# Performance work log

Measured on AMD Instinct MI355X. Metric: run time of the kernel, lower is better.

The kernel has to match this reference:

```python
import jax, jax.numpy as jnp
import numpy as np

NUM_EMBEDDINGS = 8192
EMBEDDING_DIM = 512
COMMITMENT_COST = 0.25


def setup_inputs() -> dict:
    key = jax.random.key(0)
    kz, ke = jax.random.split(key)
    z = jax.random.normal(kz, (2, EMBEDDING_DIM, 8, 32, 32), dtype=jnp.float32)
    # matches nn.Embedding init uniform_(-1/K, 1/K)
    emb_w = jax.random.uniform(
        ke, (NUM_EMBEDDINGS, EMBEDDING_DIM), dtype=jnp.float32,
        minval=-1.0 / NUM_EMBEDDINGS, maxval=1.0 / NUM_EMBEDDINGS)
    return {"z": z, "emb_w": emb_w}


def reference(z, emb_w):
    B, C, F, H, W = z.shape
    # [B,C,F,H,W] -> [N, C]
    z_flat = jnp.transpose(z, (0, 2, 3, 4, 1)).reshape(-1, C)
    # squared L2 distances via expansion: |z|^2 + |e|^2 - 2 z.e
    dist = (jnp.sum(z_flat * z_flat, axis=1, keepdims=True)
            + jnp.sum(emb_w * emb_w, axis=1)
            - 2.0 * jnp.matmul(z_flat, emb_w.T))  # [N, K]
    indices = jnp.argmin(dist, axis=1)  # [N]
    z_q_flat = emb_w[indices]  # [N, C]
    z_q = jnp.transpose(z_q_flat.reshape(B, F, H, W, C), (0, 4, 1, 2, 3))
    diff = z_q - z
    mse = jnp.mean(diff * diff)
    # codebook_loss == commitment_loss numerically (detach only affects grads)
    vq_loss = mse + COMMITMENT_COST * mse
    # straight-through estimator: value equals z_q
    z_q_ste = z + jax.lax.stop_gradient(z_q - z)
    indices = indices.reshape(B, F, H, W)
    return (z_q_ste, vq_loss, indices)
```

## Files before the change

kernel.cpp:

```cpp
#include <hip/hip_runtime.h>


constexpr int KCB = 8192;
constexpr int CD  = 512;
constexpr int SD  = 8192;
constexpr int NB  = 2;
constexpr int NR  = NB * SD;
constexpr long ZQ_ELEMS = (long)NB * CD * SD;

constexpr size_t WS_CNT   = 64;
constexpr size_t WS_KEYS  = 128;
constexpr size_t WS_RISK  = 131200;
constexpr size_t WS_IDX   = 196736;
constexpr size_t WS_LIST  = 262272;
constexpr size_t WS_ZNORM = 327808;
constexpr size_t WS_EMBT  = 458752;
constexpr size_t WS_ZH    = 17235968;
constexpr size_t WS_ZM    = 34013184;
constexpr size_t WS_EH    = 50790400;
constexpr size_t WS_EM    = 59179008;

#define RISK_EPS 2.0e-7f
#define WINDOW   1.3e-4f

constexpr int BUFB = 32768;

typedef __attribute__((ext_vector_type(8))) short short8;
typedef __attribute__((ext_vector_type(4))) float f32x4;

__device__ __forceinline__ unsigned int fkey(float f) {
  unsigned int b = __float_as_uint(f);
  return (b & 0x80000000u) ? ~b : (b | 0x80000000u);
}
__device__ __forceinline__ float unfkey(unsigned int u) {
  return (u & 0x80000000u) ? __uint_as_float(u ^ 0x80000000u)
                           : __uint_as_float(~u);
}
__device__ __forceinline__ ushort bf16_rne(float f, float* back) {
  unsigned int u = __float_as_uint(f);
  ushort h = (ushort)((u + 0x7FFFu + ((u >> 16) & 1u)) >> 16);
  *back = __uint_as_float((unsigned int)h << 16);
  return h;
}
__device__ __forceinline__ void gload16(const void* g, void* l) {
  __builtin_amdgcn_global_load_lds(
      (const __attribute__((address_space(1))) unsigned int*)g,
      (__attribute__((address_space(3))) unsigned int*)l, 16, 0, 0);
}


__global__ __launch_bounds__(256) void k_prep_z(const float* __restrict__ z,
                                                ushort* __restrict__ zh,
                                                ushort* __restrict__ zm,
                                                float* __restrict__ znorm) {
  __shared__ float t[32][65];
  int tid = threadIdx.x;
  int n0 = blockIdx.x * 64;
  int b = n0 >> 13, s0 = n0 & (SD - 1);
  int rt = n0 >> 8;
  int rowoff = n0 & 255;
  const float* zb = z + (size_t)b * CD * SD + s0;
  double a = 0.0;
  int r = tid >> 2, cs = tid & 3;
  int rtile = rowoff + r;
  int csw = cs ^ ((rtile >> 1) & 3);
  for (int ct = 0; ct < 16; ++ct) {
    __syncthreads();
    #pragma unroll
    for (int i = 0; i < 8; ++i) {
      int c = i * 4 + (tid >> 6);
      t[c][tid & 63] = zb[(size_t)(ct * 32 + c) * SD + (tid & 63)];
    }
    __syncthreads();
    union { ushort u[8]; int4 v; } ph, pm;
    #pragma unroll
    for (int j = 0; j < 8; ++j) {
      float f = t[cs * 8 + j][r];
      float fh, fm;
      ph.u[j] = bf16_rne(f, &fh);
      float r1 = f - fh;
      pm.u[j] = bf16_rne(r1, &fm);
    }
    size_t off = ((size_t)rt * 16 + ct) * 8192 + (size_t)rtile * 32 + csw * 8;
    *(int4*)(zh + off) = ph.v;
    *(int4*)(zm + off) = pm.v;
    if (tid < 64) {
      #pragma unroll
      for (int c = 0; c < 32; ++c) {
        double v = (double)t[c][tid];
        a = fma(v, v, a);
      }
    }
  }
  if (tid < 64) znorm[n0 + tid] = (float)a;
}

__global__ __launch_bounds__(256) void k_esplit(const float* __restrict__ emb,
                                                ushort* __restrict__ eh,
                                                ushort* __restrict__ em) {
  __shared__ float t[32][257];
  int rt = blockIdx.x >> 4, ct = blockIdx.x & 15;
  int k0 = rt * 256;
  #pragma unroll 4
  for (int i = 0; i < 32; ++i) {
    int idx = i * 256 + threadIdx.x;
    int r = idx >> 5, c = idx & 31;
    t[c][r] = emb[(size_t)(k0 + r) * CD + ct * 32 + c];
  }
  __syncthreads();
  size_t tbase = ((size_t)rt * 16 + ct) * 8192;
  #pragma unroll
  for (int p = 0; p < 4; ++p) {
    int slot = p * 256 + threadIdx.x;
    int r = slot >> 2, cs = slot & 3;
    int csw = cs ^ ((r >> 1) & 3);
    union { ushort u[8]; int4 v; } ph, pm;
    #pragma unroll
    for (int j = 0; j < 8; ++j) {
      float f = t[cs * 8 + j][r];
      float fh, fm;
      ph.u[j] = bf16_rne(f, &fh);
      float r1 = f - fh;
      pm.u[j] = bf16_rne(r1, &fm);
    }
    size_t off = tbase + (size_t)r * 32 + csw * 8;
    *(int4*)(eh + off) = ph.v;
    *(int4*)(em + off) = pm.v;
  }
}

__global__ __launch_bounds__(256) void k_transpose(const float* __restrict__ emb,
                                                   float* __restrict__ embt) {
  __shared__ float t[64][65];
  int bk = blockIdx.x & 127, bc = blockIdx.x >> 7;
  int k0 = bk * 64, c0 = bc * 64;
  int t4 = threadIdx.x & 15, tq = threadIdx.x >> 4;
  #pragma unroll
  for (int p = 0; p < 4; ++p) {
    int kk = p * 16 + tq;
    float4 v = *(const float4*)(emb + (size_t)(k0 + kk) * CD + c0 + 4 * t4);
    t[kk][4*t4+0] = v.x; t[kk][4*t4+1] = v.y; t[kk][4*t4+2] = v.z; t[kk][4*t4+3] = v.w;
  }
  __syncthreads();
  #pragma unroll
  for (int p = 0; p < 4; ++p) {
    int cc = p * 16 + tq;
    float4 v;
    v.x = t[4*t4+0][cc]; v.y = t[4*t4+1][cc]; v.z = t[4*t4+2][cc]; v.w = t[4*t4+3][cc];
    *(float4*)(embt + (size_t)(c0 + cc) * KCB + k0 + 4 * t4) = v;
  }
}

__global__ __launch_bounds__(256, 2) void k_dist_mfma(
    const ushort* __restrict__ zh, const ushort* __restrict__ zm,
    const ushort* __restrict__ eh, const ushort* __restrict__ em,
    const float* __restrict__ znorm,
    unsigned long long* __restrict__ keys, unsigned int* __restrict__ riskArr) {
  extern __shared__ __align__(16) char smem[];

  int tid  = threadIdx.x;
  int lane = tid & 63;
  int wid  = tid >> 6;
  int wm = wid >> 1, wn = wid & 1;
  int lk = lane >> 4, lc = lane & 15;

  int bid = (int)blockIdx.x;
  int swz = (bid & 7) * 64 + (bid >> 3);
  int mblk = swz >> 2;
  int nq   = swz & 3;
  int m0    = mblk * 128;
  int n_rt  = m0 >> 8;
  int ahalf = (m0 >> 7) & 1;

  size_t thr8 = (size_t)tid * 8;
  int    tid16 = tid * 16;

  int afo[4], bfo[4];
  #pragma unroll
  for (int mi = 0; mi < 4; ++mi) {
    int rowA = wm * 64 + mi * 16 + lc;
    afo[mi] = rowA * 64 + ((lk ^ ((rowA >> 1) & 3)) << 4);
  }
  #pragma unroll
  for (int ni = 0; ni < 4; ++ni) {
    int rowB = wn * 64 + ni * 16 + lc;
    bfo[ni] = rowB * 64 + ((lk ^ ((rowB >> 1) & 3)) << 4);
  }

  float Aab[16];
  #pragma unroll
  for (int li = 0; li < 16; ++li)
    Aab[li] = znorm[m0 + wm * 64 + (li >> 2) * 16 + lk * 4 + (li & 3)];

  unsigned long long bkey[16];
  float rminv[16];
  #pragma unroll
  for (int li = 0; li < 16; ++li) { bkey[li] = ~0ull; rminv[li] = 3.402823466e38f; }

#define STAGE(s_) do {                                                    \
    int it_ = (s_) >> 4, ks_ = (s_) & 15;                                 \
    char* lb_ = smem + ((s_) & 1) * BUFB;                                 \
    size_t ae_ = (size_t)(n_rt * 16 + ks_) * 8192 + (size_t)ahalf * 4096  \
                 + thr8;                                                  \
    size_t be_ = (size_t)((nq * 8 + (it_ >> 1)) * 16 + ks_) * 8192        \
                 + (size_t)(it_ & 1) * 4096 + thr8;                       \
    gload16(zh + ae_,        lb_ + tid16);                                \
    gload16(zh + ae_ + 2048, lb_ + 4096 + tid16);                         \
    gload16(zm + ae_,        lb_ + 8192 + tid16);                         \
    gload16(zm + ae_ + 2048, lb_ + 12288 + tid16);                        \
    gload16(eh + be_,        lb_ + 16384 + tid16);                        \
    gload16(eh + be_ + 2048, lb_ + 20480 + tid16);                        \
    gload16(em + be_,        lb_ + 24576 + tid16);                        \
    gload16(em + be_ + 2048, lb_ + 28672 + tid16);                        \
  } while (0)

  STAGE(0);

  for (int it = 0; it < 16; ++it) {
    f32x4 acc[4][4];
    #pragma unroll
    for (int mi = 0; mi < 4; ++mi)
      #pragma unroll
      for (int ni = 0; ni < 4; ++ni) {
        f32x4 zz = {0.f, 0.f, 0.f, 0.f};
        acc[mi][ni] = zz;
      }

    for (int ks = 0; ks < 16; ++ks) {
      int s = it * 16 + ks;
      __syncthreads();
      if (s + 1 < 256) STAGE(s + 1);

      const char* Cb = smem + (s & 1) * BUFB;
      short8 a_h[4], a_m[4];
      #pragma unroll
      for (int mi = 0; mi < 4; ++mi) {
        a_h[mi] = *(const short8*)(Cb + afo[mi]);
        a_m[mi] = *(const short8*)(Cb + 8192 + afo[mi]);
      }
      #pragma unroll
      for (int ni = 0; ni < 4; ++ni) {
        short8 b_h = *(const short8*)(Cb + 16384 + bfo[ni]);
        short8 b_m = *(const short8*)(Cb + 24576 + bfo[ni]);
        #pragma unroll
        for (int mi = 0; mi < 4; ++mi)
          acc[mi][ni] = __builtin_amdgcn_mfma_f32_16x16x32_bf16(a_h[mi], b_h, acc[mi][ni], 0, 0, 0);
        #pragma unroll
        for (int mi = 0; mi < 4; ++mi)
          acc[mi][ni] = __builtin_amdgcn_mfma_f32_16x16x32_bf16(a_h[mi], b_m, acc[mi][ni], 0, 0, 0);
        #pragma unroll
        for (int mi = 0; mi < 4; ++mi)
          acc[mi][ni] = __builtin_amdgcn_mfma_f32_16x16x32_bf16(a_m[mi], b_h, acc[mi][ni], 0, 0, 0);
      }
    }

    int N0 = nq * 2048 + it * 128;
    #pragma unroll
    for (int ni = 0; ni < 4; ++ni) {
      int col = N0 + wn * 64 + ni * 16 + lc;
      #pragma unroll
      for (int mi = 0; mi < 4; ++mi) {
        #pragma unroll
        for (int r = 0; r < 4; ++r) {
          int li = mi * 4 + r;
          float ab = Aab[li];
          float q  = -2.0f * acc[mi][ni][r];
          float sv = ab + q;
          float bvv = sv - ab;
          float t   = q - bvv;
          unsigned int su = __float_as_uint(sv);
          float ulp = __uint_as_float(su & 0x7f800000u) * 1.1920929e-7f;
          bool risky = (0.5f * ulp - fabsf(t)) < RISK_EPS;
          if (((su & 0x7fffffu) == 0u) && (t < 0.f))
            risky |= ((0.25f * ulp + t) < RISK_EPS);
          unsigned long long key =
              ((unsigned long long)fkey(sv) << 32) | (unsigned int)col;
          if (key < bkey[li]) bkey[li] = key;
          if (risky && sv < rminv[li]) rminv[li] = sv;
        }
      }
    }
  }
#undef STAGE

  __syncthreads();
  unsigned long long* red = (unsigned long long*)smem;
  #pragma unroll
  for (int li = 0; li < 16; ++li) {
    int row = wm * 64 + (li >> 2) * 16 + lk * 4 + (li & 3);
    red[row * 32 + wn * 16 + lc] = bkey[li];
  }
  __syncthreads();
  if (tid < 128) {
    unsigned long long mn = ~0ull;
    #pragma unroll 4
    for (int i = 0; i < 32; ++i) {
      unsigned long long v = red[tid * 32 + i];
      if (v < mn) mn = v;
    }
    atomicMin(&keys[m0 + tid], mn);
  }
  __syncthreads();
  unsigned int* red2 = (unsigned int*)smem;
  #pragma unroll
  for (int li = 0; li < 16; ++li) {
    int row = wm * 64 + (li >> 2) * 16 + lk * 4 + (li & 3);
    red2[row * 32 + wn * 16 + lc] = fkey(rminv[li]);
  }
  __syncthreads();
  if (tid < 128) {
    unsigned int mn = 0xFFFFFFFFu;
    #pragma unroll 4
    for (int i = 0; i < 32; ++i) {
      unsigned int v = red2[tid * 32 + i];
      if (v < mn) mn = v;
    }
    atomicMin(&riskArr[m0 + tid], mn);
  }
}

__global__ __launch_bounds__(256) void k_resolve(const unsigned long long* __restrict__ keys,
                                                 const unsigned int* __restrict__ riskArr,
                                                 int* __restrict__ idxArr,
                                                 int* __restrict__ list,
                                                 unsigned int* __restrict__ cnt) {
  int row = blockIdx.x * 256 + threadIdx.x;
  unsigned long long kk = keys[row];
  idxArr[row] = (int)(kk & 0xffffffffull) & (KCB - 1);
  float smin = unfkey((unsigned int)(kk >> 32));
  float rmin = unfkey(riskArr[row]);
  if (rmin <= smin + WINDOW) {
    unsigned int pos = atomicAdd(cnt, 1u);
    list[pos & (NR - 1)] = row;
  }
}

__global__ __launch_bounds__(256) void k_rescan(const float* __restrict__ z,
                                                const float* __restrict__ embt,
                                                const float* __restrict__ znorm,
                                                const int* __restrict__ list,
                                                const unsigned int* __restrict__ cnt,
                                                int* __restrict__ idxArr) {
  __shared__ float zs[512];
  __shared__ unsigned long long rk[256];
  int tid = threadIdx.x;
  unsigned int nr = *cnt;
  if (nr > (unsigned int)NR) nr = NR;
  for (unsigned int li = blockIdx.x; li < nr; li += gridDim.x) {
    int row = list[li] & (NR - 1);
    int b = row >> 13, s = row & (SD - 1);
    const float* zp = z + (size_t)b * CD * SD + s;
    zs[tid]       = zp[(size_t)tid * SD];
    zs[tid + 256] = zp[(size_t)(tid + 256) * SD];
    __syncthreads();
    float A = znorm[row];
    unsigned long long best = ~0ull;
    #pragma unroll 1
    for (int g = 0; g < 8; ++g) {
      int ka = tid + g * 1024;
      float a0 = 0.f, a1 = 0.f, a2 = 0.f, a3 = 0.f;
      #pragma unroll 8
      for (int c = 0; c < CD; ++c) {
        const float* ep = embt + (size_t)c * KCB + ka;
        float zc = zs[c];
        a0 = fmaf(zc, ep[0],   a0);
        a1 = fmaf(zc, ep[256], a1);
        a2 = fmaf(zc, ep[512], a2);
        a3 = fmaf(zc, ep[768], a3);
      }
      float av[4] = {a0, a1, a2, a3};
      #pragma unroll
      for (int jj = 0; jj < 4; ++jj) {
        int k = ka + jj * 256;
        float d = A - 2.0f * av[jj];
        unsigned long long key =
            ((unsigned long long)fkey(d) << 32) | (unsigned int)k;
        if (key < best) best = key;
      }
    }
    rk[tid] = best;
    __syncthreads();
    for (int s2 = 128; s2; s2 >>= 1) {
      if (tid < s2 && rk[tid + s2] < rk[tid]) rk[tid] = rk[tid + s2];
      __syncthreads();
    }
    if (tid == 0) idxArr[row] = (int)(rk[0] & 0xffffffffull) & (KCB - 1);
    __syncthreads();
  }
}

__global__ __launch_bounds__(256) void k_gather(const float* __restrict__ z,
                                                const float* __restrict__ emb,
                                                const int* __restrict__ idxArr,
                                                float* __restrict__ out,
                                                double* __restrict__ acc) {
  __shared__ float q[64][129];
  __shared__ int   idxs[64];
  __shared__ float wpart[4];
  int tid = threadIdx.x;
  int n0 = blockIdx.x * 64;
  int b = n0 >> 13, s0 = n0 & (SD - 1);
  if (tid < 64) {
    int idx = idxArr[n0 + tid] & (KCB - 1);
    idxs[tid] = idx;
    out[ZQ_ELEMS + 1 + n0 + tid] = (float)idx;
  }
  __syncthreads();
  int sl = tid & 63;
  int cg = tid >> 6;
  float sum = 0.f;
  const float* zb = z   + (size_t)b * CD * SD + s0 + sl;
  float*       ob = out + (size_t)b * CD * SD + s0 + sl;
  for (int cc = 0; cc < 4; ++cc) {
    int cbase = cc * 128;
    __syncthreads();
    {
      int r = tid >> 2, p = tid & 3;
      const float* e = emb + (size_t)idxs[r] * CD + cbase + p * 32;
      #pragma unroll
      for (int j = 0; j < 8; ++j) {
        float4 v = *(const float4*)(e + j * 4);
        q[r][p*32 + j*4 + 0] = v.x; q[r][p*32 + j*4 + 1] = v.y;
        q[r][p*32 + j*4 + 2] = v.z; q[r][p*32 + j*4 + 3] = v.w;
      }
    }
    __syncthreads();
    #pragma unroll 8
    for (int j = 0; j < 32; ++j) {
      int c = cbase + cg * 32 + j;
      float zv = zb[(size_t)c * SD];
      float qv = q[sl][cg * 32 + j];
      float d = qv - zv;
      sum += d * d;
      ob[(size_t)c * SD] = zv + (qv - zv);
    }
  }
  #pragma unroll
  for (int off = 32; off; off >>= 1) sum += __shfl_down(sum, off);
  if ((tid & 63) == 0) wpart[tid >> 6] = sum;
  __syncthreads();
  if (tid == 0) {
    double t = (double)wpart[0] + (double)wpart[1] + (double)wpart[2] + (double)wpart[3];
    atomicAdd(acc, t);
  }
}

__global__ void k_loss(const double* __restrict__ acc, float* __restrict__ out) {
  out[ZQ_ELEMS] = (float)(1.25 * (*acc) / (double)ZQ_ELEMS);
}

extern "C" void kernel_launch(void* const* d_in, const int* in_sizes, int n_in,
                              void* d_out, int out_size, void* d_ws, size_t ws_size,
                              hipStream_t stream) {
  const float* z   = (const float*)d_in[0];
  const float* emb = (const float*)d_in[1];
  float* out = (float*)d_out;
  double*             acc   = (double*)d_ws;
  unsigned int*       cnt   = (unsigned int*)((char*)d_ws + WS_CNT);
  unsigned long long* keys  = (unsigned long long*)((char*)d_ws + WS_KEYS);
  unsigned int*       risk  = (unsigned int*)((char*)d_ws + WS_RISK);
  int*                idxA  = (int*)((char*)d_ws + WS_IDX);
  int*                list  = (int*)((char*)d_ws + WS_LIST);
  float*              znorm = (float*)((char*)d_ws + WS_ZNORM);
  float*              embt  = (float*)((char*)d_ws + WS_EMBT);
  ushort* zh = (ushort*)((char*)d_ws + WS_ZH);
  ushort* zm = (ushort*)((char*)d_ws + WS_ZM);
  ushort* eh = (ushort*)((char*)d_ws + WS_EH);
  ushort* em = (ushort*)((char*)d_ws + WS_EM);
  (void)in_sizes; (void)n_in; (void)out_size; (void)ws_size;

  hipMemsetAsync(d_ws, 0, 128, stream);
  hipMemsetAsync((char*)d_ws + WS_KEYS, 0xFF, 196608, stream);

  k_prep_z   <<<NR / 64, 256, 0, stream>>>(z, zh, zm, znorm);
  k_esplit   <<<(KCB / 256) * 16, 256, 0, stream>>>(emb, eh, em);
  k_transpose<<<(KCB / 64) * (CD / 64), 256, 0, stream>>>(emb, embt);
  k_dist_mfma<<<512, 256, 2 * BUFB, stream>>>(zh, zm, eh, em, znorm, keys, risk);
  k_resolve  <<<NR / 256, 256, 0, stream>>>(keys, risk, idxA, list, cnt);
  k_rescan   <<<256, 256, 0, stream>>>(z, embt, znorm, list, cnt, idxA);
  k_gather   <<<NR / 64, 256, 0, stream>>>(z, emb, idxA, out, acc);
  k_loss     <<<1, 1, 0, stream>>>(acc, out);
}
```

Baseline: 652.9 us.

## Batch four rows per block in rescan and vectorize prep loads

Result: slower. 798.9 us (+22.4%).

```diff
diff --git a/kernel.cpp b/kernel.cpp
--- a/kernel.cpp
+++ b/kernel.cpp
@@ -53,7 +53,7 @@
                                                 ushort* __restrict__ zh,
                                                 ushort* __restrict__ zm,
                                                 float* __restrict__ znorm) {
-  __shared__ float t[32][65];
+  __shared__ float t[32][68];
   int tid = threadIdx.x;
   int n0 = blockIdx.x * 64;
   int b = n0 >> 13, s0 = n0 & (SD - 1);
@@ -67,9 +67,11 @@
   for (int ct = 0; ct < 16; ++ct) {
     __syncthreads();
     #pragma unroll
-    for (int i = 0; i < 8; ++i) {
-      int c = i * 4 + (tid >> 6);
-      t[c][tid & 63] = zb[(size_t)(ct * 32 + c) * SD + (tid & 63)];
+    for (int i = 0; i < 2; ++i) {
+      int idx = i * 256 + tid;
+      int c = idx >> 4, l = idx & 15;
+      float4 v = *(const float4*)(zb + (size_t)(ct * 32 + c) * SD + l * 4);
+      *(float4*)&t[c][l * 4] = v;
     }
     __syncthreads();
     union { ushort u[8]; int4 v; } ph, pm;
@@ -101,11 +103,13 @@
   __shared__ float t[32][257];
   int rt = blockIdx.x >> 4, ct = blockIdx.x & 15;
   int k0 = rt * 256;
-  #pragma unroll 4
-  for (int i = 0; i < 32; ++i) {
+  #pragma unroll
+  for (int i = 0; i < 8; ++i) {
     int idx = i * 256 + threadIdx.x;
-    int r = idx >> 5, c = idx & 31;
-    t[c][r] = emb[(size_t)(k0 + r) * CD + ct * 32 + c];
+    int r = idx >> 3, f4i = idx & 7;
+    float4 v = *(const float4*)(emb + (size_t)(k0 + r) * CD + ct * 32 + f4i * 4);
+    t[f4i*4+0][r] = v.x; t[f4i*4+1][r] = v.y;
+    t[f4i*4+2][r] = v.z; t[f4i*4+3][r] = v.w;
   }
   __syncthreads();
   size_t tbase = ((size_t)rt * 16 + ct) * 8192;
@@ -341,51 +345,79 @@
                                                 const int* __restrict__ list,
                                                 const unsigned int* __restrict__ cnt,
                                                 int* __restrict__ idxArr) {
-  __shared__ float zs[512];
+  __shared__ float zs[4][512];
+  __shared__ float As[4];
   __shared__ unsigned long long rk[256];
   int tid = threadIdx.x;
   unsigned int nr = *cnt;
   if (nr > (unsigned int)NR) nr = NR;
-  for (unsigned int li = blockIdx.x; li < nr; li += gridDim.x) {
-    int row = list[li] & (NR - 1);
-    int b = row >> 13, s = row & (SD - 1);
-    const float* zp = z + (size_t)b * CD * SD + s;
-    zs[tid]       = zp[(size_t)tid * SD];
-    zs[tid + 256] = zp[(size_t)(tid + 256) * SD];
+  for (unsigned int base = blockIdx.x * 4; base < nr; base += gridDim.x * 4) {
+    int nrow = (int)(nr - base); if (nrow > 4) nrow = 4;
     __syncthreads();
-    float A = znorm[row];
-    unsigned long long best = ~0ull;
+    #pragma unroll
+    for (int r = 0; r < 4; ++r) {
+      if (r < nrow) {
+        int row = list[base + r] & (NR - 1);
+        int b = row >> 13, s = row & (SD - 1);
+        const float* zp = z + (size_t)b * CD * SD + s;
+        zs[r][tid]       = zp[(size_t)tid * SD];
+        zs[r][tid + 256] = zp[(size_t)(tid + 256) * SD];
+        if (tid == 0) As[r] = znorm[row];
+      } else {
+        zs[r][tid] = 0.f; zs[r][tid + 256] = 0.f;
+        if (tid == 0) As[r] = 0.f;
+      }
+    }
+    __syncthreads();
+    unsigned long long best[4];
+    #pragma unroll
+    for (int r = 0; r < 4; ++r) best[r] = ~0ull;
     #pragma unroll 1
     for (int g = 0; g < 8; ++g) {
       int ka = tid + g * 1024;
-      float a0 = 0.f, a1 = 0.f, a2 = 0.f, a3 = 0.f;
-      #pragma unroll 8
+      float acc[4][4];
+      #pragma unroll
+      for (int r = 0; r < 4; ++r)
+        #pragma unroll
+        for (int j = 0; j < 4; ++j) acc[r][j] = 0.f;
+      #pragma unroll 4
       for (int c = 0; c < CD; ++c) {
         const float* ep = embt + (size_t)c * KCB + ka;
-        float zc = zs[c];
-        a0 = fmaf(zc, ep[0],   a0);
-        a1 = fmaf(zc, ep[256], a1);
-        a2 = fmaf(zc, ep[512], a2);
-        a3 = fmaf(zc, ep[768], a3);
-      }
-      float av[4] = {a0, a1, a2, a3};
+        float e0 = ep[0], e1 = ep[256], e2 = ep[512], e3 = ep[768];
+        #pragma unroll
+        for (int r = 0; r < 4; ++r) {
+          float zc = zs[r][c];
+          acc[r][0] = fmaf(zc, e0, acc[r][0]);
+          acc[r][1] = fmaf(zc, e1, acc[r][1]);
+          acc[r][2] = fmaf(zc, e2, acc[r][2]);
+          acc[r][3] = fmaf(zc, e3, acc[r][3]);
+        }
+      }
       #pragma unroll
       for (int jj = 0; jj < 4; ++jj) {
         int k = ka + jj * 256;
-        float d = A - 2.0f * av[jj];
-        unsigned long long key =
-            ((unsigned long long)fkey(d) << 32) | (unsigned int)k;
-        if (key < best) best = key;
-      }
-    }
-    rk[tid] = best;
-    __syncthreads();
-    for (int s2 = 128; s2; s2 >>= 1) {
-      if (tid < s2 && rk[tid + s2] < rk[tid]) rk[tid] = rk[tid + s2];
+        #pragma unroll
+        for (int r = 0; r < 4; ++r) {
+          float d = As[r] - 2.0f * acc[r][jj];
+          unsigned long long key =
+              ((unsigned long long)fkey(d) << 32) | (unsigned int)k;
+          if (key < best[r]) best[r] = key;
+        }
+      }
+    }
+    for (int r = 0; r < nrow; ++r) {
       __syncthreads();
-    }
-    if (tid == 0) idxArr[row] = (int)(rk[0] & 0xffffffffull) & (KCB - 1);
-    __syncthreads();
+      rk[tid] = best[r];
+      __syncthreads();
+      for (int s2 = 128; s2; s2 >>= 1) {
+        if (tid < s2 && rk[tid + s2] < rk[tid]) rk[tid] = rk[tid + s2];
+        __syncthreads();
+      }
+      if (tid == 0) {
+        int row = list[base + r] & (NR - 1);
+        idxArr[row] = (int)(rk[0] & 0xffffffffull) & (KCB - 1);
+      }
+    }
   }
 }
 
@@ -477,7 +509,7 @@
   k_transpose<<<(KCB / 64) * (CD / 64), 256, 0, stream>>>(emb, embt);
   k_dist_mfma<<<512, 256, 2 * BUFB, stream>>>(zh, zm, eh, em, znorm, keys, risk);
   k_resolve  <<<NR / 256, 256, 0, stream>>>(keys, risk, idxA, list, cnt);
-  k_rescan   <<<256, 256, 0, stream>>>(z, embt, znorm, list, cnt, idxA);
+  k_rescan   <<<128, 256, 0, stream>>>(z, embt, znorm, list, cnt, idxA);
   k_gather   <<<NR / 64, 256, 0, stream>>>(z, emb, idxA, out, acc);
   k_loss     <<<1, 1, 0, stream>>>(acc, out);
 }
```

## Load codebook MFMA fragments directly from global, stage only z tiles in LDS

Applied to the files above, without the earlier changes.

Result: slower. 675.4 us (+3.4%).

```diff
diff --git a/kernel.cpp b/kernel.cpp
--- a/kernel.cpp
+++ b/kernel.cpp
@@ -23,7 +23,7 @@
 #define RISK_EPS 2.0e-7f
 #define WINDOW   1.3e-4f
 
-constexpr int BUFB = 32768;
+constexpr int BUFB = 16384;
 
 typedef __attribute__((ext_vector_type(8))) short short8;
 typedef __attribute__((ext_vector_type(4))) float f32x4;
@@ -156,7 +156,7 @@
     const ushort* __restrict__ eh, const ushort* __restrict__ em,
     const float* __restrict__ znorm,
     unsigned long long* __restrict__ keys, unsigned int* __restrict__ riskArr) {
-  extern __shared__ __align__(16) char smem[];
+  __shared__ __align__(16) char smem[2 * BUFB];
 
   int tid  = threadIdx.x;
   int lane = tid & 63;
@@ -175,7 +175,8 @@
   size_t thr8 = (size_t)tid * 8;
   int    tid16 = tid * 16;
 
-  int afo[4], bfo[4];
+  int afo[4];
+  size_t bfoU[4];
   #pragma unroll
   for (int mi = 0; mi < 4; ++mi) {
     int rowA = wm * 64 + mi * 16 + lc;
@@ -184,37 +185,26 @@
   #pragma unroll
   for (int ni = 0; ni < 4; ++ni) {
     int rowB = wn * 64 + ni * 16 + lc;
-    bfo[ni] = rowB * 64 + ((lk ^ ((rowB >> 1) & 3)) << 4);
-  }
-
-  float Aab[16];
-  #pragma unroll
-  for (int li = 0; li < 16; ++li)
-    Aab[li] = znorm[m0 + wm * 64 + (li >> 2) * 16 + lk * 4 + (li & 3)];
+    bfoU[ni] = (size_t)rowB * 32 + ((lk ^ ((rowB >> 1) & 3)) << 3);
+  }
 
   unsigned long long bkey[16];
   float rminv[16];
   #pragma unroll
   for (int li = 0; li < 16; ++li) { bkey[li] = ~0ull; rminv[li] = 3.402823466e38f; }
 
-#define STAGE(s_) do {                                                    \
-    int it_ = (s_) >> 4, ks_ = (s_) & 15;                                 \
+#define STAGE_A(s_) do {                                                  \
+    int ks_ = (s_) & 15;                                                  \
     char* lb_ = smem + ((s_) & 1) * BUFB;                                 \
     size_t ae_ = (size_t)(n_rt * 16 + ks_) * 8192 + (size_t)ahalf * 4096  \
                  + thr8;                                                  \
-    size_t be_ = (size_t)((nq * 8 + (it_ >> 1)) * 16 + ks_) * 8192        \
-                 + (size_t)(it_ & 1) * 4096 + thr8;                       \
     gload16(zh + ae_,        lb_ + tid16);                                \
     gload16(zh + ae_ + 2048, lb_ + 4096 + tid16);                         \
     gload16(zm + ae_,        lb_ + 8192 + tid16);                         \
     gload16(zm + ae_ + 2048, lb_ + 12288 + tid16);                        \
-    gload16(eh + be_,        lb_ + 16384 + tid16);                        \
-    gload16(eh + be_ + 2048, lb_ + 20480 + tid16);                        \
-    gload16(em + be_,        lb_ + 24576 + tid16);                        \
-    gload16(em + be_ + 2048, lb_ + 28672 + tid16);                        \
   } while (0)
 
-  STAGE(0);
+  STAGE_A(0);
 
   for (int it = 0; it < 16; ++it) {
     f32x4 acc[4][4];
@@ -229,7 +219,15 @@
     for (int ks = 0; ks < 16; ++ks) {
       int s = it * 16 + ks;
       __syncthreads();
-      if (s + 1 < 256) STAGE(s + 1);
+      if (s + 1 < 256) STAGE_A(s + 1);
+
+      size_t bOff = (size_t)((nq * 8 + (it >> 1)) * 16 + ks) * 8192
+                  + (size_t)(it & 1) * 4096;
+      short8 b_h[4], b_m[4];
+      #pragma unroll
+      for (int ni = 0; ni < 4; ++ni) b_h[ni] = *(const short8*)(eh + bOff + bfoU[ni]);
+      #pragma unroll
+      for (int ni = 0; ni < 4; ++ni) b_m[ni] = *(const short8*)(em + bOff + bfoU[ni]);
 
       const char* Cb = smem + (s & 1) * BUFB;
       short8 a_h[4], a_m[4];
@@ -240,17 +238,15 @@
       }
       #pragma unroll
       for (int ni = 0; ni < 4; ++ni) {
-        short8 b_h = *(const short8*)(Cb + 16384 + bfo[ni]);
-        short8 b_m = *(const short8*)(Cb + 24576 + bfo[ni]);
         #pragma unroll
         for (int mi = 0; mi < 4; ++mi)
-          acc[mi][ni] = __builtin_amdgcn_mfma_f32_16x16x32_bf16(a_h[mi], b_h, acc[mi][ni], 0, 0, 0);
+          acc[mi][ni] = __builtin_amdgcn_mfma_f32_16x16x32_bf16(a_h[mi], b_h[ni], acc[mi][ni], 0, 0, 0);
         #pragma unroll
         for (int mi = 0; mi < 4; ++mi)
-          acc[mi][ni] = __builtin_amdgcn_mfma_f32_16x16x32_bf16(a_h[mi], b_m, acc[mi][ni], 0, 0, 0);
+          acc[mi][ni] = __builtin_amdgcn_mfma_f32_16x16x32_bf16(a_h[mi], b_m[ni], acc[mi][ni], 0, 0, 0);
         #pragma unroll
         for (int mi = 0; mi < 4; ++mi)
-          acc[mi][ni] = __builtin_amdgcn_mfma_f32_16x16x32_bf16(a_m[mi], b_h, acc[mi][ni], 0, 0, 0);
+          acc[mi][ni] = __builtin_amdgcn_mfma_f32_16x16x32_bf16(a_m[mi], b_h[ni], acc[mi][ni], 0, 0, 0);
       }
     }
 
@@ -260,10 +256,14 @@
       int col = N0 + wn * 64 + ni * 16 + lc;
       #pragma unroll
       for (int mi = 0; mi < 4; ++mi) {
+        float A4[4];
+        #pragma unroll
+        for (int r = 0; r < 4; ++r)
+          A4[r] = znorm[m0 + wm * 64 + mi * 16 + lk * 4 + r];
         #pragma unroll
         for (int r = 0; r < 4; ++r) {
           int li = mi * 4 + r;
-          float ab = Aab[li];
+          float ab = A4[r];
           float q  = -2.0f * acc[mi][ni][r];
           float sv = ab + q;
           float bvv = sv - ab;
@@ -281,7 +281,7 @@
       }
     }
   }
-#undef STAGE
+#undef STAGE_A
 
   __syncthreads();
   unsigned long long* red = (unsigned long long*)smem;
@@ -475,7 +475,7 @@
   k_prep_z   <<<NR / 64, 256, 0, stream>>>(z, zh, zm, znorm);
   k_esplit   <<<(KCB / 256) * 16, 256, 0, stream>>>(emb, eh, em);
   k_transpose<<<(KCB / 64) * (CD / 64), 256, 0, stream>>>(emb, embt);
-  k_dist_mfma<<<512, 256, 2 * BUFB, stream>>>(zh, zm, eh, em, znorm, keys, risk);
+  k_dist_mfma<<<512, 256, 0, stream>>>(zh, zm, eh, em, znorm, keys, risk);
   k_resolve  <<<NR / 256, 256, 0, stream>>>(keys, risk, idxA, list, cnt);
   k_rescan   <<<256, 256, 0, stream>>>(z, embt, znorm, list, cnt, idxA);
   k_gather   <<<NR / 64, 256, 0, stream>>>(z, emb, idxA, out, acc);
```
